# Kernel optimization log

Hardware: AMD Instinct MI355X
Metric: run time of the kernel (lower is better)

## Reference

```python
import jax, jax.numpy as jnp
import numpy as np

VOCAB = 32000
HID = 1024
LAYERS = 6
HEADS = 8 * 2  # 16
HEAD_DIM = HID // HEADS
INTER = int(HID * 8 / 3)  # 2730, matches torch int(hidden*8/3)
MAX_POS = 2048
EPS = 1e-5


def setup_inputs() -> dict:
    key = jax.random.key(0)
    ks = jax.random.split(key, 16)
    B, S = 2, 1024
    input_ids = jax.random.randint(ks[0], (B, S), 0, VOCAB)

    def lin(k, out_d, in_d, stack=True):
        shape = (LAYERS, out_d, in_d) if stack else (out_d, in_d)
        return jax.random.normal(k, shape, jnp.float32) * (in_d ** -0.5)

    return {
        "input_ids": input_ids,
        "tok_emb": jax.random.normal(ks[1], (VOCAB, HID), jnp.float32) * 0.02,
        "pos_emb": jax.random.normal(ks[2], (MAX_POS, HID), jnp.float32) * 0.02,
        "qkv_w": lin(ks[3], 3 * HID, HID),
        "o_w": lin(ks[4], HID, HID),
        "gate_w": lin(ks[5], INTER, HID),
        "up_w": lin(ks[6], INTER, HID),
        "down_w": lin(ks[7], HID, INTER),
        "ln1_w": jnp.ones((LAYERS, HID), jnp.float32),
        "ln1_b": jnp.zeros((LAYERS, HID), jnp.float32),
        "ln2_w": jnp.ones((LAYERS, HID), jnp.float32),
        "ln2_b": jnp.zeros((LAYERS, HID), jnp.float32),
        "lnf_w": jnp.ones((HID,), jnp.float32),
        "lnf_b": jnp.zeros((HID,), jnp.float32),
        "head_w": lin(ks[8], VOCAB, HID, stack=False),
    }


def _layernorm(x, w, b):
    mu = jnp.mean(x, axis=-1, keepdims=True)
    var = jnp.mean(jnp.square(x - mu), axis=-1, keepdims=True)
    return (x - mu) * jax.lax.rsqrt(var + EPS) * w + b


def _forward(input_ids, tok_emb, pos_emb, qkv_w, o_w, gate_w, up_w, down_w,
             ln1_w, ln1_b, ln2_w, ln2_b, lnf_w, lnf_b, head_w):
    B, S = input_ids.shape
    h = tok_emb[input_ids] + pos_emb[jnp.arange(S)][None, :, :]  # [B,S,H]
    scale = HEAD_DIM ** -0.5

    def layer(h, p):
        qkv_w, o_w, gate_w, up_w, down_w, l1w, l1b, l2w, l2b = p
        # attention block
        x = _layernorm(h, l1w, l1b)
        qkv = jnp.einsum('bsh,oh->bso', x, qkv_w)  # [B,S,3H]
        qkv = qkv.reshape(B, S, 3, HEADS, HEAD_DIM)
        q, k, v = qkv[:, :, 0], qkv[:, :, 1], qkv[:, :, 2]  # [B,S,Hn,Dh]
        attn = jnp.einsum('bqnd,bknd->bnqk', q, k) * scale  # [B,Hn,S,S]
        attn = jax.nn.softmax(attn, axis=-1)
        ctx = jnp.einsum('bnqk,bknd->bqnd', attn, v).reshape(B, S, HID)
        h = h + jnp.einsum('bsh,oh->bso', ctx, o_w)
        # MLP block (SwiGLU)
        x = _layernorm(h, l2w, l2b)
        gate = jax.nn.silu(jnp.einsum('bsh,ih->bsi', x, gate_w))
        up = jnp.einsum('bsh,ih->bsi', x, up_w)
        h = h + jnp.einsum('bsi,hi->bsh', gate * up, down_w)
        return h, None

    h, _ = jax.lax.scan(layer, h, (qkv_w, o_w, gate_w, up_w, down_w,
                                   ln1_w, ln1_b, ln2_w, ln2_b))
    h = _layernorm(h, lnf_w, lnf_b)
    logits = jnp.einsum('bsh,vh->bsv', h, head_w)  # [B,S,V]
    return logits


def reference(input_ids, tok_emb, pos_emb, qkv_w, o_w, gate_w, up_w, down_w,
              ln1_w, ln1_b, ln2_w, ln2_b, lnf_w, lnf_b, head_w):
    return _forward(input_ids, tok_emb, pos_emb, qkv_w, o_w, gate_w, up_w,
                    down_w, ln1_w, ln1_b, ln2_w, ln2_b, lnf_w, lnf_b, head_w)
```

## Files before the change

kernel.cpp:

```cpp
#include <hip/hip_runtime.h>

typedef unsigned short u16;
typedef __attribute__((ext_vector_type(8))) short bf16x8;
typedef __attribute__((ext_vector_type(8))) unsigned short us8;
typedef __attribute__((ext_vector_type(4))) unsigned short us4;
typedef __attribute__((ext_vector_type(4))) float f32x4;

#define SEQ    1024
#define TOK    2048
#define HID    1024
#define NLAYER 6
#define NHEAD  16
#define HDIM   64
#define QKV3   3072
#define INTER  2730
#define IPAD   2816
#define VOCAB  32000
#define LN_EPS 1e-5f

__device__ __forceinline__ u16 f2bf(float f) {
  unsigned u = __float_as_uint(f);
  return (u16)((u + 0x7fffu + ((u >> 16) & 1u)) >> 16);
}
__device__ __forceinline__ float bf2f(u16 u) {
  return __uint_as_float(((unsigned)u) << 16);
}

__device__ __forceinline__ void gl_lds16(const void* g, void* l) {
  __builtin_amdgcn_global_load_lds(
      (const __attribute__((address_space(1))) void*)g,
      (__attribute__((address_space(3))) void*)l, 16, 0, 0);
}

__global__ __launch_bounds__(256) void embed_kernel(
    const int* __restrict__ ids, const float* __restrict__ tok,
    const float* __restrict__ pos, float* __restrict__ h)
{
  int t = blockIdx.x;
  int s = t & (SEQ - 1);
  int id = ids[t];
  int c = threadIdx.x * 4;
  float4 tv = *(const float4*)(tok + (long)id * HID + c);
  float4 pv = *(const float4*)(pos + (long)s * HID + c);
  float4 o;
  o.x = tv.x + pv.x; o.y = tv.y + pv.y; o.z = tv.z + pv.z; o.w = tv.w + pv.w;
  *(float4*)(h + (long)t * HID + c) = o;
}

__device__ __forceinline__ void ln_body(
    int t, int tid, const float* __restrict__ h, const float* __restrict__ w,
    const float* __restrict__ b, u16* __restrict__ out, float* r1, float* r2)
{
  int lane = tid & 63, wid = tid >> 6;
  float4 v = *(const float4*)(h + (long)t * HID + tid * 4);
  float s1 = v.x + v.y + v.z + v.w;
  float s2 = v.x * v.x + v.y * v.y + v.z * v.z + v.w * v.w;
#pragma unroll
  for (int o = 32; o > 0; o >>= 1) { s1 += __shfl_down(s1, o); s2 += __shfl_down(s2, o); }
  if (lane == 0) { r1[wid] = s1; r2[wid] = s2; }
  __syncthreads();
  float t1 = r1[0] + r1[1] + r1[2] + r1[3];
  float t2 = r2[0] + r2[1] + r2[2] + r2[3];
  float mu = t1 * (1.f / HID);
  float var = t2 * (1.f / HID) - mu * mu;
  float rs = rsqrtf(var + LN_EPS);
  float4 wv = *(const float4*)(w + tid * 4);
  float4 bv = *(const float4*)(b + tid * 4);
  us4 o4;
  o4[0] = f2bf((v.x - mu) * rs * wv.x + bv.x);
  o4[1] = f2bf((v.y - mu) * rs * wv.y + bv.y);
  o4[2] = f2bf((v.z - mu) * rs * wv.z + bv.z);
  o4[3] = f2bf((v.w - mu) * rs * wv.w + bv.w);
  *(us4*)(out + (long)t * HID + tid * 4) = o4;
}

__global__ __launch_bounds__(256) void ln_kernel(
    const float* __restrict__ h, const float* __restrict__ w,
    const float* __restrict__ b, u16* __restrict__ out)
{
  __shared__ float r1[4], r2[4];
  ln_body(blockIdx.x, threadIdx.x, h, w, b, out, r1, r2);
}

__global__ __launch_bounds__(256) void pre1_kernel(
    const float* __restrict__ h, const float* __restrict__ lw,
    const float* __restrict__ lb, u16* __restrict__ x,
    const float* __restrict__ qkv_w, u16* __restrict__ wq)
{
  __shared__ float r1[4], r2[4];
  int bid = blockIdx.x;
  if (bid < 2048) {
    ln_body(bid, threadIdx.x, h, lw, lb, x, r1, r2);
    return;
  }
  long i = (long)(bid - 2048) * 256 + threadIdx.x;
  const float* s = qkv_w + i * 8;
  us8 o;
#pragma unroll
  for (int j = 0; j < 8; ++j) o[j] = f2bf(s[j]);
  *(us8*)(wq + i * 8) = o;
}

__global__ __launch_bounds__(256) void fin_kernel(
    const float* __restrict__ h, const float* __restrict__ lw,
    const float* __restrict__ lb, u16* __restrict__ x,
    const float* __restrict__ head_w, u16* __restrict__ whead)
{
  __shared__ float r1[4], r2[4];
  int bid = blockIdx.x;
  if (bid < 2048) {
    ln_body(bid, threadIdx.x, h, lw, lb, x, r1, r2);
    return;
  }
  long i = (long)(bid - 2048) * 256 + threadIdx.x;
  const float* s = head_w + i * 8;
  us8 o;
#pragma unroll
  for (int j = 0; j < 8; ++j) o[j] = f2bf(s[j]);
  *(us8*)(whead + i * 8) = o;
}

__global__ __launch_bounds__(256, 3) void attn_cvt_kernel(
    const u16* __restrict__ qkv, const u16* __restrict__ vT,
    u16* __restrict__ ctx,
    const float* __restrict__ o_w, const float* __restrict__ gate,
    const float* __restrict__ up, const float* __restrict__ down,
    const float* __restrict__ next_qkv_w,
    u16* __restrict__ wo, u16* __restrict__ wgu, u16* __restrict__ wd,
    u16* __restrict__ wq)
{
  __shared__ u16 Ks[8][128][8];
  __shared__ u16 Vs[16][64][8];
  __shared__ u16 Ps[4][16 * 128];

  const int bid = blockIdx.x;
  const int tid = threadIdx.x;

  if (bid >= 512) {
    long i = (long)(bid - 512) * 256 + tid;
    us8 o;
    if (i < 131072L) {
      const float* s = o_w + i * 8;
#pragma unroll
      for (int j = 0; j < 8; ++j) o[j] = f2bf(s[j]);
      *(us8*)(wo + i * 8) = o;
    } else if (i < 851968L) {
      long i3 = i - 131072L;
      int n = (int)(i3 >> 7);
      int kc = (int)(i3 & 127);
      int g = n >> 1;
      const float* s = (n & 1) ? up : gate;
#pragma unroll
      for (int j = 0; j < 8; ++j) {
        int k = kc * 8 + j;
        o[j] = f2bf((g < INTER) ? s[(long)g * HID + k] : 0.f);
      }
      *(us8*)(wgu + i3 * 8) = o;
    } else if (i < 1212416L) {
      long i4 = i - 851968L;
      int n = (int)(i4 / 352);
      int kc = (int)(i4 % 352);
#pragma unroll
      for (int j = 0; j < 8; ++j) {
        int k = kc * 8 + j;
        o[j] = f2bf((k < INTER) ? down[(long)n * INTER + k] : 0.f);
      }
      *(us8*)(wd + i4 * 8) = o;
    } else {
      long i5 = i - 1212416L;
      const float* s = next_qkv_w + i5 * 8;
#pragma unroll
      for (int j = 0; j < 8; ++j) o[j] = f2bf(s[j]);
      *(us8*)(wq + i5 * 8) = o;
    }
    return;
  }

  const int lane = tid & 63;
  const int w    = tid >> 6;
  const int lo   = lane & 15;
  const int hi   = lane >> 4;

  const int z  = bid & 31;
  const int qt = bid >> 5;
  const int b  = z >> 4, h = z & 15;

  const u16* Qb  = qkv + (long)b * SEQ * QKV3 + h * 64;
  const u16* Kb  = Qb + 1024;
  const u16* Vtb = vT + (long)z * 65536;

  bf16x8 q[2];
#pragma unroll
  for (int ks = 0; ks < 2; ++ks)
    q[ks] = *(const bf16x8*)(Qb + (long)(qt * 64 + w * 16 + lo) * QKV3 + ks * 32 + hi * 8);

  f32x4 po[4];
  float m_run[4], l_run[4];
#pragma unroll
  for (int r = 0; r < 4; ++r) { m_run[r] = -1e30f; l_run[r] = 0.f; }
#pragma unroll
  for (int nd = 0; nd < 4; ++nd) po[nd] = (f32x4){0.f, 0.f, 0.f, 0.f};

  char* Pw = (char*)&Ps[w][0];

  for (int c = 0; c < 8; ++c) {
#pragma unroll
    for (int i = 0; i < 4; ++i) {
      int u = w * 4 + i, g = u & 7, rg = u >> 3;
      gl_lds16(Kb + (long)(c * 128 + rg * 64 + lane) * QKV3 + g * 8, &Ks[g][rg * 64][0]);
    }
#pragma unroll
    for (int i = 0; i < 4; ++i) {
      int kg = w * 4 + i;
      gl_lds16(Vtb + (long)lane * 1024 + c * 128 + kg * 8, &Vs[kg][0][0]);
    }
    __syncthreads();

    f32x4 s[8];
#pragma unroll
    for (int jf = 0; jf < 8; ++jf) s[jf] = (f32x4){0.f, 0.f, 0.f, 0.f};
#pragma unroll
    for (int jf = 0; jf < 8; ++jf) {
      bf16x8 bk[2];
#pragma unroll
      for (int ks = 0; ks < 2; ++ks)
        bk[ks] = *(const bf16x8*)&Ks[ks * 4 + hi][jf * 16 + lo][0];
#pragma unroll
      for (int ks = 0; ks < 2; ++ks)
        s[jf] = __builtin_amdgcn_mfma_f32_16x16x32_bf16(q[ks], bk[ks], s[jf], 0, 0, 0);
    }

    float scf[4];
#pragma unroll
    for (int r = 0; r < 4; ++r) {
      float rm = -1e30f;
#pragma unroll
      for (int jf = 0; jf < 8; ++jf) {
        s[jf][r] *= 0.125f;
        rm = fmaxf(rm, s[jf][r]);
      }
#pragma unroll
      for (int o = 1; o < 16; o <<= 1) rm = fmaxf(rm, __shfl_xor(rm, o));
      float mn = fmaxf(m_run[r], rm);
      float sc = __expf(m_run[r] - mn);
      float rs = 0.f;
#pragma unroll
      for (int jf = 0; jf < 8; ++jf) {
        float e = __expf(s[jf][r] - mn);
        s[jf][r] = e;
        rs += e;
      }
#pragma unroll
      for (int o = 1; o < 16; o <<= 1) rs += __shfl_xor(rs, o);
      l_run[r] = l_run[r] * sc + rs;
      m_run[r] = mn;
      scf[r] = sc;
    }

#pragma unroll
    for (int jf = 0; jf < 8; ++jf)
#pragma unroll
      for (int r = 0; r < 4; ++r) {
        int row = hi * 4 + r;
        int byo = row * 256 + ((((jf * 16 + lo) * 2)) ^ ((row & 7) << 4));
        *(u16*)(Pw + byo) = f2bf(s[jf][r]);
      }
#pragma unroll
    for (int nd = 0; nd < 4; ++nd)
#pragma unroll
      for (int r = 0; r < 4; ++r) po[nd][r] *= scf[r];

    bf16x8 pa[4];
#pragma unroll
    for (int ks2 = 0; ks2 < 4; ++ks2) {
      int row = lo;
      int byo = row * 256 + (((ks2 * 32 + hi * 8) * 2) ^ ((row & 7) << 4));
      pa[ks2] = *(const bf16x8*)(Pw + byo);
    }
#pragma unroll
    for (int nd = 0; nd < 4; ++nd) {
      bf16x8 bv[4];
#pragma unroll
      for (int ks2 = 0; ks2 < 4; ++ks2)
        bv[ks2] = *(const bf16x8*)&Vs[ks2 * 4 + hi][nd * 16 + lo][0];
#pragma unroll
      for (int ks2 = 0; ks2 < 4; ++ks2)
        po[nd] = __builtin_amdgcn_mfma_f32_16x16x32_bf16(pa[ks2], bv[ks2], po[nd], 0, 0, 0);
    }
    __syncthreads();
  }

#pragma unroll
  for (int r = 0; r < 4; ++r) {
    float inv = 1.f / l_run[r];
    int qrow = qt * 64 + w * 16 + hi * 4 + r;
    u16* dst = ctx + (long)(b * SEQ + qrow) * HID + h * 64;
#pragma unroll
    for (int nd = 0; nd < 4; ++nd)
      dst[nd * 16 + lo] = f2bf(po[nd][r] * inv);
  }
}

template<int BM, int BN, int EPI>
__global__ __launch_bounds__(256) void gemm_bt(
    const u16* __restrict__ A, const u16* __restrict__ B,
    void* __restrict__ Cv, const float* __restrict__ resid,
    int lda, int ldb, int ldc, int K, float scale, int bdiv,
    long sA1, long sA2, long sB1, long sB2, long sC1, long sC2)
{
  constexpr int FM = BM / 32;
  constexpr int FN = BN / 32;
  constexpr int TRW = 136;
  constexpr int SMEMU = (EPI == 4 && 128 * TRW > 2 * (BM + BN) * 32)
                        ? 128 * TRW : 2 * (BM + BN) * 32;
  __shared__ u16 smem[SMEMU];
  auto absb = [&](int buf) { return smem + buf * (BM * 32); };
  auto bsb  = [&](int buf) { return smem + 2 * (BM * 32) + buf * (BN * 32); };

  const int tid = threadIdx.x;
  const int lane = tid & 63;
  const int wid = tid >> 6;
  const int wm = wid >> 1, wn = wid & 1;

  const int z = blockIdx.z;
  const long offA = (long)(z / bdiv) * sA1 + (long)(z % bdiv) * sA2;
  const long offB = (long)(z / bdiv) * sB1 + (long)(z % bdiv) * sB2;
  const long offC = (long)(z / bdiv) * sC1 + (long)(z % bdiv) * sC2;

  const u16* Ab = A + offA + (long)blockIdx.x * BM * lda;
  const u16* Bb = B + offB + (long)blockIdx.y * BN * ldb;

  auto stage = [&](int buf, int kt) {
    const u16* a = Ab + (long)kt * 32;
    const u16* bsrc = Bb + (long)kt * 32;
#pragma unroll
    for (int i = 0; i < BM / 64; ++i) {
      int row = i * 64 + wid * 16 + (lane >> 2);
      gl_lds16(a + (long)row * lda + (lane & 3) * 8, absb(buf) + i * 2048 + wid * 512);
    }
#pragma unroll
    for (int i = 0; i < BN / 64; ++i) {
      int row = i * 64 + wid * 16 + (lane >> 2);
      gl_lds16(bsrc + (long)row * ldb + (lane & 3) * 8, bsb(buf) + i * 2048 + wid * 512);
    }
  };

  f32x4 acc[FM][FN];
#pragma unroll
  for (int i = 0; i < FM; ++i)
#pragma unroll
    for (int j = 0; j < FN; ++j) acc[i][j] = (f32x4){0.f, 0.f, 0.f, 0.f};

  int aoff[FM], boff[FN];
#pragma unroll
  for (int i = 0; i < FM; ++i)
    aoff[i] = (wm * (BM / 2) + i * 16 + (lane & 15)) * 32 + (lane >> 4) * 8;
#pragma unroll
  for (int j = 0; j < FN; ++j)
    boff[j] = (wn * (BN / 2) + j * 16 + (lane & 15)) * 32 + (lane >> 4) * 8;

  const int KT = K >> 5;
  stage(0, 0);
  __syncthreads();
  int cur = 0;
  for (int kt = 0; kt < KT; ++kt) {
    if (kt + 1 < KT) stage(cur ^ 1, kt + 1);
    bf16x8 av[FM], bv[FN];
#pragma unroll
    for (int i = 0; i < FM; ++i) av[i] = *(const bf16x8*)(absb(cur) + aoff[i]);
#pragma unroll
    for (int j = 0; j < FN; ++j) bv[j] = *(const bf16x8*)(bsb(cur) + boff[j]);
#pragma unroll
    for (int i = 0; i < FM; ++i)
#pragma unroll
      for (int j = 0; j < FN; ++j)
        acc[i][j] = __builtin_amdgcn_mfma_f32_16x16x32_bf16(av[i], bv[j], acc[i][j], 0, 0, 0);
    __syncthreads();
    cur ^= 1;
  }

  const int r0 = blockIdx.x * BM + wm * (BM / 2) + (lane >> 4) * 4;
  const int c0 = blockIdx.y * BN + wn * (BN / 2) + (lane & 15);

  if (EPI == 4 && blockIdx.y >= 16) {
    u16* Tr = smem;
    const int clb = wn * 64 + (lane & 15);
    const int rlb = wm * 64 + (lane >> 4) * 4;
#pragma unroll
    for (int i = 0; i < FM; ++i) {
#pragma unroll
      for (int j = 0; j < FN; ++j) {
        us4 t4;
#pragma unroll
        for (int r = 0; r < 4; ++r) t4[r] = f2bf(acc[i][j][r]);
        *(us4*)(Tr + (clb + j * 16) * TRW + rlb + i * 16) = t4;
      }
    }
    __syncthreads();
    const int bb  = blockIdx.x >> 3;
    const int k0  = (blockIdx.x & 7) * 128;
    const int vcb = blockIdx.y * 128 - 2048;
    const int c_loc = tid >> 1, half = tid & 1;
    const int vcol = vcb + c_loc;
    u16* vTo = (u16*)(void*)resid;
    u16* dst = vTo + (long)(bb * 16 + (vcol >> 6)) * 65536
             + (long)(vcol & 63) * 1024 + k0 + half * 64;
    const u16* srcl = Tr + c_loc * TRW + half * 64;
#pragma unroll
    for (int j = 0; j < 8; ++j)
      *(us8*)(dst + j * 8) = *(const us8*)(srcl + j * 8);
    return;
  }

#pragma unroll
  for (int i = 0; i < FM; ++i) {
#pragma unroll
    for (int j = 0; j < FN; ++j) {
      f32x4 v = acc[i][j];
#pragma unroll
      for (int r = 0; r < 4; ++r) {
        if (EPI == 3) {
          float pv = __shfl_xor(v[r], 1);
          if ((lane & 1) == 0) {
            float gf = v[r];
            float res = gf / (1.f + __expf(-gf)) * pv;
            int cc = c0 + j * 16;
            long idx = offC + (long)(r0 + i * 16 + r) * ldc + (cc >> 1);
            ((u16*)Cv)[idx] = f2bf(res);
          }
        } else {
          long idx = offC + (long)(r0 + i * 16 + r) * ldc + (c0 + j * 16);
          if (EPI == 0 || EPI == 4) ((u16*)Cv)[idx] = f2bf(v[r] * scale);
          else if (EPI == 1)        ((float*)Cv)[idx] = v[r] * scale;
          else                      ((float*)Cv)[idx] = resid[idx] + v[r];
        }
      }
    }
  }
}

template<int EPI>
__global__ __launch_bounds__(512, 1) void gemm256(
    const u16* __restrict__ A, const u16* __restrict__ B,
    void* __restrict__ Cv, int NB, int ldc)
{
  __shared__ u16 lds[2][2][2][8][128][8];

  const int tid  = threadIdx.x;
  const int lane = tid & 63;
  const int w    = tid >> 6;
  const int wm   = w >> 2;
  const int wn   = w & 3;
  const int arow = lane & 15;
  const int kg   = lane >> 4;

  const int flat = blockIdx.x;
  const int swz  = (flat & 7) * NB + (flat >> 3);
  const int bm   = swz & 7;
  const int bn   = swz >> 3;

  const u16* Ab = A + (long)bm * 256 * 1024;
  const u16* Bb = B + (long)bn * 256 * 1024;

  auto stage = [&](int mat, int d, int half, int t) {
#pragma unroll
    for (int i = 0; i < 2; ++i) {
      const int u  = w * 2 + i;
      const int g  = u & 7;
      const int rg = u >> 3;
      const u16* src = (mat == 0 ? Ab : Bb)
                     + (long)(half * 128 + rg * 64 + lane) * 1024 + t * 64 + g * 8;
      gl_lds16(src, &lds[d][mat][half][g][rg * 64][0]);
    }
  };

  f32x4 acc[2][2][4][2];
#pragma unroll
  for (int qm = 0; qm < 2; ++qm)
#pragma unroll
    for (int qn = 0; qn < 2; ++qn)
#pragma unroll
      for (int f = 0; f < 4; ++f)
#pragma unroll
        for (int n = 0; n < 2; ++n) acc[qm][qn][f][n] = (f32x4){0.f, 0.f, 0.f, 0.f};

  bf16x8 a[4][2];
  bf16x8 b[2][2][2];

  auto rdA = [&](int d, int qm) {
#pragma unroll
    for (int f = 0; f < 4; ++f)
#pragma unroll
      for (int ks = 0; ks < 2; ++ks)
        a[f][ks] = *(const bf16x8*)&lds[d][0][wm][ks * 4 + kg][qm * 64 + f * 16 + arow][0];
  };
  auto rdB = [&](int d, int qn) {
#pragma unroll
    for (int n = 0; n < 2; ++n)
#pragma unroll
      for (int ks = 0; ks < 2; ++ks)
        b[qn][n][ks] = *(const bf16x8*)&lds[d][1][wn >> 1][ks * 4 + kg]
                                          [(wn & 1) * 64 + qn * 32 + n * 16 + arow][0];
  };
  auto mm = [&](int qm, int qn) {
#pragma unroll
    for (int f = 0; f < 4; ++f)
#pragma unroll
      for (int n = 0; n < 2; ++n)
#pragma unroll
        for (int ks = 0; ks < 2; ++ks)
          acc[qm][qn][f][n] = __builtin_amdgcn_mfma_f32_16x16x32_bf16(
              a[f][ks], b[qn][n][ks], acc[qm][qn][f][n], 0, 0, 0);
  };

#define BAR asm volatile("s_barrier" ::: "memory")
#define PRIO1 __builtin_amdgcn_s_setprio(1)
#define PRIO0 __builtin_amdgcn_s_setprio(0)

  stage(1, 0, 0, 0);
  stage(0, 0, 0, 0);
  stage(0, 0, 1, 0);
  stage(1, 0, 1, 0);
  stage(1, 1, 0, 1);
  stage(0, 1, 0, 1);
  asm volatile("s_waitcnt vmcnt(4)" ::: "memory");
  BAR;

  const int iters = 8;
#pragma unroll 1
  for (int it = 0; it < iters; ++it) {
    const int T = 2 * it;
    const bool pf = (it + 1 < iters);
    rdA(0, 0); rdB(0, 0); rdB(0, 1);
    stage(0, 1, 1, T + 1);
    stage(1, 1, 1, T + 1);
    BAR; PRIO1; mm(0, 0); mm(0, 1); PRIO0; BAR;
    rdA(0, 1);
    if (pf) { stage(1, 0, 0, T + 2);
              stage(0, 0, 0, T + 2); }
    BAR; PRIO1; mm(1, 0); mm(1, 1); PRIO0;
    if (pf) asm volatile("s_waitcnt vmcnt(4)" ::: "memory");
    else    asm volatile("s_waitcnt vmcnt(0)" ::: "memory");
    BAR;
    rdA(1, 0); rdB(1, 0); rdB(1, 1);
    if (pf) { stage(0, 0, 1, T + 2);
              stage(1, 0, 1, T + 2); }
    BAR; PRIO1; mm(0, 0); mm(0, 1); PRIO0; BAR;
    rdA(1, 1);
    if (pf) { stage(1, 1, 0, T + 3);
              stage(0, 1, 0, T + 3); }
    BAR; PRIO1; mm(1, 0); mm(1, 1); PRIO0;
    if (pf) asm volatile("s_waitcnt vmcnt(4)" ::: "memory");
    BAR;
  }
#undef BAR
#undef PRIO1
#undef PRIO0

#pragma unroll
  for (int qm = 0; qm < 2; ++qm) {
#pragma unroll
    for (int qn = 0; qn < 2; ++qn) {
#pragma unroll
      for (int f = 0; f < 4; ++f) {
        const int r0 = bm * 256 + wm * 128 + qm * 64 + f * 16 + kg * 4;
#pragma unroll
        for (int n = 0; n < 2; ++n) {
          const int c = bn * 256 + wn * 64 + qn * 32 + n * 16 + arow;
          f32x4 v = acc[qm][qn][f][n];
#pragma unroll
          for (int r = 0; r < 4; ++r) {
            long idx = (long)(r0 + r) * ldc + c;
            if (EPI == 0) ((u16*)Cv)[idx] = f2bf(v[r]);
            else          ((float*)Cv)[idx] = v[r];
          }
        }
      }
    }
  }
}

extern "C" void kernel_launch(void* const* d_in, const int* in_sizes, int n_in,
                              void* d_out, int out_size, void* d_ws, size_t ws_size,
                              hipStream_t stream)
{
  (void)in_sizes; (void)n_in; (void)out_size; (void)ws_size;
  const int*   ids     = (const int*)d_in[0];
  const float* tok_emb = (const float*)d_in[1];
  const float* pos_emb = (const float*)d_in[2];
  const float* qkv_w   = (const float*)d_in[3];
  const float* o_w     = (const float*)d_in[4];
  const float* gate_w  = (const float*)d_in[5];
  const float* up_w    = (const float*)d_in[6];
  const float* down_w  = (const float*)d_in[7];
  const float* ln1_w   = (const float*)d_in[8];
  const float* ln1_b   = (const float*)d_in[9];
  const float* ln2_w   = (const float*)d_in[10];
  const float* ln2_b   = (const float*)d_in[11];
  const float* lnf_w   = (const float*)d_in[12];
  const float* lnf_b   = (const float*)d_in[13];
  const float* head_w  = (const float*)d_in[14];

  char* ws = (char*)d_ws;
  long off = 0;
  auto alloc = [&](long bytes) { void* p = ws + off; off += (bytes + 1023) & ~1023L; return p; };
  float* h   = (float*)alloc((long)TOK * HID * 4);
  u16*   x   = (u16*)  alloc((long)TOK * HID * 2);
  u16*   qkv = (u16*)  alloc((long)TOK * QKV3 * 2);
  u16*   vT  = (u16*)  alloc(32L * HDIM * SEQ * 2);
  u16*   ctx = (u16*)  alloc((long)TOK * HID * 2);
  u16*   y   = (u16*)  alloc((long)TOK * IPAD * 2);
  u16*   whead = (u16*)alloc((long)VOCAB * HID * 2);
  u16* wq  = whead;
  u16* wo  = wq + 3072 * 1024;
  u16* wgu = wo + 1024 * 1024;
  u16* wd  = wgu + 5632 * 1024;

  embed_kernel<<<TOK, 256, 0, stream>>>(ids, tok_emb, pos_emb, h);

  for (int l = 0; l < NLAYER; ++l) {
    if (l == 0) {
      pre1_kernel<<<3584, 256, 0, stream>>>(
          h, ln1_w, ln1_b, x, qkv_w, wq);
    } else {
      ln_kernel<<<TOK, 256, 0, stream>>>(h, ln1_w + l * HID, ln1_b + l * HID, x);
    }

    gemm_bt<128, 128, 4><<<dim3(16, 24, 1), 256, 0, stream>>>(
        x, wq, qkv, (const float*)vT, HID, HID, QKV3, HID, 1.f, 1, 0, 0, 0, 0, 0, 0);

    const int cvt_blocks = (l + 1 < NLAYER) ? 6272 : 4736;
    attn_cvt_kernel<<<dim3(512 + cvt_blocks), 256, 0, stream>>>(
        qkv, vT, ctx,
        o_w + (long)l * HID * HID,
        gate_w + (long)l * INTER * HID, up_w + (long)l * INTER * HID,
        down_w + (long)l * HID * INTER,
        qkv_w + (long)(l + 1 < NLAYER ? l + 1 : l) * QKV3 * HID,
        wo, wgu, wd, wq);

    gemm_bt<64, 128, 2><<<dim3(32, 8, 1), 256, 0, stream>>>(
        ctx, wo, h, h, HID, HID, HID, HID, 1.f, 1, 0, 0, 0, 0, 0, 0);

    ln_kernel<<<TOK, 256, 0, stream>>>(h, ln2_w + l * HID, ln2_b + l * HID, x);

    gemm_bt<128, 128, 3><<<dim3(16, 44, 1), 256, 0, stream>>>(
        x, wgu, y, nullptr, HID, HID, IPAD, HID, 1.f, 1, 0, 0, 0, 0, 0, 0);

    gemm_bt<64, 128, 2><<<dim3(32, 8, 1), 256, 0, stream>>>(
        y, wd, h, h, IPAD, IPAD, HID, IPAD, 1.f, 1, 0, 0, 0, 0, 0, 0);
  }

  fin_kernel<<<18048, 256, 0, stream>>>(h, lnf_w, lnf_b, x, head_w, whead);
  gemm256<1><<<dim3(1000), 512, 0, stream>>>(x, whead, d_out, 125, VOCAB);
}
```

Before: 1.206 ms.

## Redistribute per-layer weight conversions across GEMM kernels as extra blocks

Moves the fp32-to-bf16 weight conversion work out of the attention kernel and spreads it over the GEMM launches as extra trailing blocks. The o_proj weights are converted alongside the QKV GEMM, down weights alongside the o-proj GEMM, and next-layer QKV weights alongside the gate/up GEMM, with only gate/up remaining in the attention kernel. The goal is to balance the memory-bound conversion against compute-bound GEMMs so that fewer cycles are spent idle. In exchange the GEMM kernels lose the unused batched-stride support and gain a branch. Conversion blocks may also compete with GEMM blocks for CU slots.

Result: slower. 1.236 ms (+2.5%).

```diff
diff --git a/kernel.cpp b/kernel.cpp
--- a/kernel.cpp
+++ b/kernel.cpp
@@ -30,6 +30,37 @@
   __builtin_amdgcn_global_load_lds(
       (const __attribute__((address_space(1))) void*)g,
       (__attribute__((address_space(3))) void*)l, 16, 0, 0);
+}
+
+__device__ __forceinline__ void cvt_slice(
+    long i, int mode, const float* __restrict__ s1,
+    const float* __restrict__ s2, u16* __restrict__ dst)
+{
+  us8 o;
+  if (mode == 0) {
+    const float* s = s1 + i * 8;
+#pragma unroll
+    for (int j = 0; j < 8; ++j) o[j] = f2bf(s[j]);
+  } else if (mode == 1) {
+    int n = (int)(i >> 7);
+    int kc = (int)(i & 127);
+    int g = n >> 1;
+    const float* s = (n & 1) ? s2 : s1;
+#pragma unroll
+    for (int j = 0; j < 8; ++j) {
+      int k = kc * 8 + j;
+      o[j] = f2bf((g < INTER) ? s[(long)g * HID + k] : 0.f);
+    }
+  } else {
+    int n = (int)(i / 352);
+    int kc = (int)(i % 352);
+#pragma unroll
+    for (int j = 0; j < 8; ++j) {
+      int k = kc * 8 + j;
+      o[j] = f2bf((k < INTER) ? s1[(long)n * INTER + k] : 0.f);
+    }
+  }
+  *(us8*)(dst + i * 8) = o;
 }
 
 __global__ __launch_bounds__(256) void embed_kernel(
@@ -94,11 +125,7 @@
     return;
   }
   long i = (long)(bid - 2048) * 256 + threadIdx.x;
-  const float* s = qkv_w + i * 8;
-  us8 o;
-#pragma unroll
-  for (int j = 0; j < 8; ++j) o[j] = f2bf(s[j]);
-  *(us8*)(wq + i * 8) = o;
+  cvt_slice(i, 0, qkv_w, nullptr, wq);
 }
 
 __global__ __launch_bounds__(256) void fin_kernel(
@@ -113,21 +140,14 @@
     return;
   }
   long i = (long)(bid - 2048) * 256 + threadIdx.x;
-  const float* s = head_w + i * 8;
-  us8 o;
-#pragma unroll
-  for (int j = 0; j < 8; ++j) o[j] = f2bf(s[j]);
-  *(us8*)(whead + i * 8) = o;
+  cvt_slice(i, 0, head_w, nullptr, whead);
 }
 
 __global__ __launch_bounds__(256, 3) void attn_cvt_kernel(
     const u16* __restrict__ qkv, const u16* __restrict__ vT,
     u16* __restrict__ ctx,
-    const float* __restrict__ o_w, const float* __restrict__ gate,
-    const float* __restrict__ up, const float* __restrict__ down,
-    const float* __restrict__ next_qkv_w,
-    u16* __restrict__ wo, u16* __restrict__ wgu, u16* __restrict__ wd,
-    u16* __restrict__ wq)
+    const float* __restrict__ gate, const float* __restrict__ up,
+    u16* __restrict__ wgu)
 {
   __shared__ u16 Ks[8][128][8];
   __shared__ u16 Vs[16][64][8];
@@ -138,41 +158,7 @@
 
   if (bid >= 512) {
     long i = (long)(bid - 512) * 256 + tid;
-    us8 o;
-    if (i < 131072L) {
-      const float* s = o_w + i * 8;
-#pragma unroll
-      for (int j = 0; j < 8; ++j) o[j] = f2bf(s[j]);
-      *(us8*)(wo + i * 8) = o;
-    } else if (i < 851968L) {
-      long i3 = i - 131072L;
-      int n = (int)(i3 >> 7);
-      int kc = (int)(i3 & 127);
-      int g = n >> 1;
-      const float* s = (n & 1) ? up : gate;
-#pragma unroll
-      for (int j = 0; j < 8; ++j) {
-        int k = kc * 8 + j;
-        o[j] = f2bf((g < INTER) ? s[(long)g * HID + k] : 0.f);
-      }
-      *(us8*)(wgu + i3 * 8) = o;
-    } else if (i < 1212416L) {
-      long i4 = i - 851968L;
-      int n = (int)(i4 / 352);
-      int kc = (int)(i4 % 352);
-#pragma unroll
-      for (int j = 0; j < 8; ++j) {
-        int k = kc * 8 + j;
-        o[j] = f2bf((k < INTER) ? down[(long)n * INTER + k] : 0.f);
-      }
-      *(us8*)(wd + i4 * 8) = o;
-    } else {
-      long i5 = i - 1212416L;
-      const float* s = next_qkv_w + i5 * 8;
-#pragma unroll
-      for (int j = 0; j < 8; ++j) o[j] = f2bf(s[j]);
-      *(us8*)(wq + i5 * 8) = o;
-    }
+    if (i < 720896L) cvt_slice(i, 1, gate, up, wgu);
     return;
   }
 
@@ -305,8 +291,9 @@
 __global__ __launch_bounds__(256) void gemm_bt(
     const u16* __restrict__ A, const u16* __restrict__ B,
     void* __restrict__ Cv, const float* __restrict__ resid,
-    int lda, int ldb, int ldc, int K, float scale, int bdiv,
-    long sA1, long sA2, long sB1, long sB2, long sC1, long sC2)
+    int lda, int ldb, int ldc, int K, float scale,
+    int mx, const float* __restrict__ cvt_s1, const float* __restrict__ cvt_s2,
+    u16* __restrict__ cvt_dst, long cvt_n, int cvt_mode)
 {
   constexpr int FM = BM / 32;
   constexpr int FN = BN / 32;
@@ -318,17 +305,20 @@
   auto bsb  = [&](int buf) { return smem + 2 * (BM * 32) + buf * (BN * 32); };
 
   const int tid = threadIdx.x;
+
+  if ((int)blockIdx.x >= mx) {
+    long id = (long)(blockIdx.x - mx) * gridDim.y + blockIdx.y;
+    long i = id * 256 + tid;
+    if (i < cvt_n) cvt_slice(i, cvt_mode, cvt_s1, cvt_s2, cvt_dst);
+    return;
+  }
+
   const int lane = tid & 63;
   const int wid = tid >> 6;
   const int wm = wid >> 1, wn = wid & 1;
 
-  const int z = blockIdx.z;
-  const long offA = (long)(z / bdiv) * sA1 + (long)(z % bdiv) * sA2;
-  const long offB = (long)(z / bdiv) * sB1 + (long)(z % bdiv) * sB2;
-  const long offC = (long)(z / bdiv) * sC1 + (long)(z % bdiv) * sC2;
-
-  const u16* Ab = A + offA + (long)blockIdx.x * BM * lda;
-  const u16* Bb = B + offB + (long)blockIdx.y * BN * ldb;
+  const u16* Ab = A + (long)blockIdx.x * BM * lda;
+  const u16* Bb = B + (long)blockIdx.y * BN * ldb;
 
   auto stage = [&](int buf, int kt) {
     const u16* a = Ab + (long)kt * 32;
@@ -425,11 +415,11 @@
             float gf = v[r];
             float res = gf / (1.f + __expf(-gf)) * pv;
             int cc = c0 + j * 16;
-            long idx = offC + (long)(r0 + i * 16 + r) * ldc + (cc >> 1);
+            long idx = (long)(r0 + i * 16 + r) * ldc + (cc >> 1);
             ((u16*)Cv)[idx] = f2bf(res);
           }
         } else {
-          long idx = offC + (long)(r0 + i * 16 + r) * ldc + (c0 + j * 16);
+          long idx = (long)(r0 + i * 16 + r) * ldc + (c0 + j * 16);
           if (EPI == 0 || EPI == 4) ((u16*)Cv)[idx] = f2bf(v[r] * scale);
           else if (EPI == 1)        ((float*)Cv)[idx] = v[r] * scale;
           else                      ((float*)Cv)[idx] = resid[idx] + v[r];
@@ -620,34 +610,38 @@
 
   for (int l = 0; l < NLAYER; ++l) {
     if (l == 0) {
-      pre1_kernel<<<3584, 256, 0, stream>>>(
-          h, ln1_w, ln1_b, x, qkv_w, wq);
+      pre1_kernel<<<3584, 256, 0, stream>>>(h, ln1_w, ln1_b, x, qkv_w, wq);
     } else {
       ln_kernel<<<TOK, 256, 0, stream>>>(h, ln1_w + l * HID, ln1_b + l * HID, x);
     }
 
-    gemm_bt<128, 128, 4><<<dim3(16, 24, 1), 256, 0, stream>>>(
-        x, wq, qkv, (const float*)vT, HID, HID, QKV3, HID, 1.f, 1, 0, 0, 0, 0, 0, 0);
-
-    const int cvt_blocks = (l + 1 < NLAYER) ? 6272 : 4736;
-    attn_cvt_kernel<<<dim3(512 + cvt_blocks), 256, 0, stream>>>(
+    gemm_bt<128, 128, 4><<<dim3(38, 24, 1), 256, 0, stream>>>(
+        x, wq, qkv, (const float*)vT, HID, HID, QKV3, HID, 1.f,
+        16, o_w + (long)l * HID * HID, nullptr, wo, 131072L, 0);
+
+    attn_cvt_kernel<<<dim3(3328), 256, 0, stream>>>(
         qkv, vT, ctx,
-        o_w + (long)l * HID * HID,
-        gate_w + (long)l * INTER * HID, up_w + (long)l * INTER * HID,
-        down_w + (long)l * HID * INTER,
-        qkv_w + (long)(l + 1 < NLAYER ? l + 1 : l) * QKV3 * HID,
-        wo, wgu, wd, wq);
+        gate_w + (long)l * INTER * HID, up_w + (long)l * INTER * HID, wgu);
+
+    gemm_bt<64, 128, 2><<<dim3(208, 8, 1), 256, 0, stream>>>(
+        ctx, wo, h, h, HID, HID, HID, HID, 1.f,
+        32, down_w + (long)l * HID * INTER, nullptr, wd, 360448L, 2);
+
+    ln_kernel<<<TOK, 256, 0, stream>>>(h, ln2_w + l * HID, ln2_b + l * HID, x);
+
+    if (l + 1 < NLAYER) {
+      gemm_bt<128, 128, 3><<<dim3(51, 44, 1), 256, 0, stream>>>(
+          x, wgu, y, nullptr, HID, HID, IPAD, HID, 1.f,
+          16, qkv_w + (long)(l + 1) * QKV3 * HID, nullptr, wq, 393216L, 0);
+    } else {
+      gemm_bt<128, 128, 3><<<dim3(16, 44, 1), 256, 0, stream>>>(
+          x, wgu, y, nullptr, HID, HID, IPAD, HID, 1.f,
+          16, nullptr, nullptr, nullptr, 0L, 0);
+    }
 
     gemm_bt<64, 128, 2><<<dim3(32, 8, 1), 256, 0, stream>>>(
-        ctx, wo, h, h, HID, HID, HID, HID, 1.f, 1, 0, 0, 0, 0, 0, 0);
-
-    ln_kernel<<<TOK, 256, 0, stream>>>(h, ln2_w + l * HID, ln2_b + l * HID, x);
-
-    gemm_bt<128, 128, 3><<<dim3(16, 44, 1), 256, 0, stream>>>(
-        x, wgu, y, nullptr, HID, HID, IPAD, HID, 1.f, 1, 0, 0, 0, 0, 0, 0);
-
-    gemm_bt<64, 128, 2><<<dim3(32, 8, 1), 256, 0, stream>>>(
-        y, wd, h, h, IPAD, IPAD, HID, IPAD, 1.f, 1, 0, 0, 0, 0, 0, 0);
+        y, wd, h, h, IPAD, IPAD, HID, IPAD, 1.f,
+        32, nullptr, nullptr, nullptr, 0L, 0);
   }
 
   fin_kernel<<<18048, 256, 0, stream>>>(h, lnf_w, lnf_b, x, head_w, whead);
```
